# Kernel tuning notes

Hardware: AMD Instinct MI355X
Metric: run time of the kernel (lower is better)

The kernel has to match this reference:

```python
import jax, jax.numpy as jnp
import numpy as np

B, T, D, H, LORA = 4, 1024, 1024, 16, 64
HD = D // H
BLOCK_ID, N_BLOCKS = 6, 12


def _ln(x, w, b, eps=1e-5):
    m = x.mean(-1, keepdims=True)
    v = ((x - m) ** 2).mean(-1, keepdims=True)
    return (x - m) * jax.lax.rsqrt(v + eps) * w + b


def _lora(z, a, b, l):
    return l + jnp.tanh(z @ a.T) @ b.T


def setup_inputs() -> dict:
    key = jax.random.key(0)
    ks = iter(jax.random.split(key, 64))
    rn = lambda shape, s: jax.random.normal(next(ks), shape, jnp.float32) * s
    inp = {}
    inp['x'] = rn((B, T, D), 1.0)
    r1 = 1.0 - BLOCK_ID / N_BLOCKS
    i = np.arange(D)
    inp['xw'] = jnp.asarray(1.0 - (i / D) ** r1, jnp.float32)
    for nm in ('rW', 'kW', 'vW', 'gW'):
        inp[nm] = rn((D, D), 0.02)
    for p in ('r', 'k', 'v', 'g', 'd'):
        inp[p + '_la'] = rn((LORA, D), 0.001)
        inp[p + '_lb'] = rn((D, LORA), 0.001)
        inp[p + '_ll'] = rn((D,), 1.0)
    inp['ln_w'] = jnp.full((HD,), ((1 + BLOCK_ID) / N_BLOCKS) ** 0.7, jnp.float32)
    inp['ln_b'] = jnp.zeros((HD,), jnp.float32)
    inp['oW'] = rn((D, D), 0.02)
    inp['init_state'] = rn((H, HD, HD), 1.0)
    r0 = BLOCK_ID / (N_BLOCKS - 1)
    ih = i % HD
    inp['u'] = jnp.asarray(r0 * (1 - ih / (D - 1)) + np.remainder(0.1 * (ih + 1), 3.0), jnp.float32)
    return inp


def reference(x, xw, rW, kW, vW, gW, r_la, r_lb, r_ll, k_la, k_lb, k_ll,
              v_la, v_lb, v_ll, g_la, g_lb, g_ll, d_la, d_lb, d_ll,
              ln_w, ln_b, oW, init_state, u):
    b, t, d = x.shape
    h = init_state.shape[0]
    hd = d // h
    # token shift: xx[t] = x[t-1], xx[0] = 0
    xx = jnp.concatenate([jnp.zeros_like(x[:, :1]), x[:, :-1]], axis=1)
    dx = xx - x
    lerpx = x + dx * xw
    r = (x + dx * _lora(lerpx, r_la, r_lb, r_ll)) @ rW.T
    k = (x + dx * _lora(lerpx, k_la, k_lb, k_ll)) @ kW.T
    v = (x + dx * _lora(lerpx, v_la, v_lb, v_ll)) @ vW.T
    g = (x + dx * _lora(lerpx, g_la, g_lb, g_ll)) @ gW.T
    w = jnp.exp(-jnp.exp(_lora(x + dx * _lora(lerpx, d_la, d_lb, d_ll), d_la, d_lb, d_ll)))
    # [B,T,D] -> [T,B,H,hd] for the time scan
    split = lambda z: z.reshape(b, t, h, hd).transpose(1, 0, 2, 3)
    rs, ws, ks, vs = split(r), split(w), split(k), split(v)
    uh = u.reshape(h, hd)
    st0 = jnp.broadcast_to(init_state, (b, h, hd, hd))

    def step(st, inp):
        rt, wt, kt, vt = inp
        kv = jnp.einsum('bhi,bhj->bhij', kt, vt)      # outer product
        y = jnp.einsum('bhi,bhij->bhj', rt, st + uh[None, :, :, None] * kv)
        return wt[..., None] * st + kv, y             # diag(w) @ S + kv

    st1, ys = jax.lax.scan(step, st0, (rs, ws, ks, vs))  # ys: [T,B,H,hd]
    o = jax.nn.silu(g.reshape(b, t, h, hd)) * _ln(ys.transpose(1, 0, 2, 3), ln_w, ln_b)
    return o.reshape(b, t, d) @ oW.T, st1
```

## Files before the change

### kernel.cpp

```cpp
#include <hip/hip_runtime.h>
#include <hip/hip_bf16.h>

typedef unsigned short u16;
typedef unsigned int u32;
typedef __attribute__((ext_vector_type(4))) float f32x4;
typedef __attribute__((ext_vector_type(8))) short s16x8;

#define AS1 __attribute__((address_space(1)))
#define AS3 __attribute__((address_space(3)))

#define NB 4
#define TTOK 1024
#define DD 1024
#define NH 16
#define HD 64
#define MT 4096
#define NCH 16
#define CLEN 64

static __device__ __forceinline__ float b2f(u16 u) {
  union { unsigned int u; float f; } c; c.u = ((unsigned int)u) << 16; return c.f;
}
static __device__ __forceinline__ u16 f2b(float f) {
  union { float f; unsigned int u; } c; c.f = f;
  return (u16)((c.u + 0x7fffu + ((c.u >> 16) & 1u)) >> 16);
}
static __device__ __forceinline__ float rdl(float v, int i) {
  union { float f; int s; } c; c.f = v;
  union { int s; float f; } o; o.s = __builtin_amdgcn_readlane(c.s, i);
  return o.f;
}
static __device__ __forceinline__ void gload16(const u16* g, u16* l) {
  __builtin_amdgcn_global_load_lds((const AS1 u32*)g, (AS3 u32*)l, 16, 0, 0);
}
static __device__ __forceinline__ int swz(int lin) {
  return lin ^ (((lin >> 9) & 3) << 5) ^ (((lin >> 7) & 1) << 4);
}

__global__ __launch_bounds__(256) void convW(const float* __restrict__ s0, const float* __restrict__ s1,
                                             const float* __restrict__ s2, const float* __restrict__ s3,
                                             const float* __restrict__ s4, u16* __restrict__ dst) {
  long f = ((long)blockIdx.x * 256 + threadIdx.x) << 2;
  int sel = (int)(f >> 20);
  const float* s = sel == 0 ? s0 : sel == 1 ? s1 : sel == 2 ? s2 : sel == 3 ? s3 : s4;
  long off = f & 1048575;
  f32x4 v = *(const f32x4*)&s[off];
  ushort4 o; o.x = f2b(v[0]); o.y = f2b(v[1]); o.z = f2b(v[2]); o.w = f2b(v[3]);
  *(ushort4*)&dst[f] = o;
}

__global__ __launch_bounds__(256) void convLora(
    const float* a0, const float* a1, const float* a2, const float* a3, const float* a4,
    const float* b0, const float* b1, const float* b2, const float* b3, const float* b4,
    const float* l0, const float* l1, const float* l2, const float* l3, const float* l4,
    u16* __restrict__ laD, u16* __restrict__ lbD, float* __restrict__ llD) {
  long f = ((long)blockIdx.x * 256 + threadIdx.x) << 2;
  if (f < 327680) {
    int sel = (int)(f >> 16); long off = f & 65535;
    const float* s = sel == 0 ? a0 : sel == 1 ? a1 : sel == 2 ? a2 : sel == 3 ? a3 : a4;
    f32x4 v = *(const f32x4*)&s[off];
    ushort4 o; o.x = f2b(v[0]); o.y = f2b(v[1]); o.z = f2b(v[2]); o.w = f2b(v[3]);
    *(ushort4*)&laD[f] = o;
  } else if (f < 655360) {
    long g = f - 327680;
    int sel = (int)(g >> 16); long off = g & 65535;
    const float* s = sel == 0 ? b0 : sel == 1 ? b1 : sel == 2 ? b2 : sel == 3 ? b3 : b4;
    f32x4 v = *(const f32x4*)&s[off];
    ushort4 o; o.x = f2b(v[0]); o.y = f2b(v[1]); o.z = f2b(v[2]); o.w = f2b(v[3]);
    *(ushort4*)&lbD[g] = o;
  } else if (f < 660480) {
    long g = f - 655360;
    int sel = (int)(g >> 10); long off = g & 1023;
    const float* s = sel == 0 ? l0 : sel == 1 ? l1 : sel == 2 ? l2 : sel == 3 ? l3 : l4;
    *(f32x4*)&llD[g] = *(const f32x4*)&s[off];
  }
}

__global__ __launch_bounds__(256) void prep(const float* __restrict__ x, const float* __restrict__ xw,
                                            u16* __restrict__ lerpx, float* __restrict__ dxP) {
  long f = ((long)blockIdx.x * 256 + threadIdx.x) << 2;
  int d = (int)(f & (DD - 1));
  int m = (int)(f >> 10);
  int t = m & (TTOK - 1);
  f32x4 xv = *(const f32x4*)&x[f];
  f32x4 xm = {};
  if (t > 0) xm = *(const f32x4*)&x[f - DD];
  f32x4 xwv = *(const f32x4*)&xw[d];
  f32x4 dx = xm - xv;
  f32x4 lp = xv + dx * xwv;
  *(f32x4*)&dxP[f] = dx;
  ushort4 o; o.x = f2b(lp[0]); o.y = f2b(lp[1]); o.z = f2b(lp[2]); o.w = f2b(lp[3]);
  *(ushort4*)&lerpx[f] = o;
}

template<int BM, int BN, int EPI>
__launch_bounds__(256)
__global__ void gemm2(const u16* __restrict__ Ab, long sAz,
                      const u16* __restrict__ Bb, long sBz,
                      void* __restrict__ Ob, long sOz,
                      const float* __restrict__ llb,
                      const float* __restrict__ xP,
                      const float* __restrict__ dxP,
                      int M, int N, int K) {
  __shared__ __align__(16) u16 As[BM * 64];
  __shared__ __align__(16) u16 Bs[BN * 64];
  const int z = blockIdx.z;
  const u16* A = Ab + (long)z * sAz;
  const u16* Bw = Bb + (long)z * sBz;
  const int m0 = blockIdx.y * BM;
  const int n0 = blockIdx.x * BN;
  const int tid = threadIdx.x;
  const int l = tid & 63;
  const int wv = tid >> 6;
  constexpr int WM = BM / 2, WN = BN / 2;
  constexpr int FM = WM / 16, FN = WN / 16;
  const int wm0 = (wv >> 1) * WM, wn0 = (wv & 1) * WN;
  const int lrow = l & 15, lk = (l >> 4) * 8;
  constexpr int GA = BM / 32, GB = BN / 32;
  int gA[GA], gB[GB];
#pragma unroll
  for (int q = 0; q < GA; ++q) {
    int d = (q * 256 + tid) * 16;
    int bb = swz(d);
    gA[q] = (m0 + (bb >> 7)) * K + ((bb & 127) >> 1);
  }
#pragma unroll
  for (int q = 0; q < GB; ++q) {
    int d = (q * 256 + tid) * 16;
    int bb = swz(d);
    gB[q] = (n0 + (bb >> 7)) * K + ((bb & 127) >> 1);
  }
  int aOff[FM][2], bOff[FN][2];
#pragma unroll
  for (int m = 0; m < FM; ++m)
#pragma unroll
    for (int kk = 0; kk < 2; ++kk)
      aOff[m][kk] = swz(((wm0 + m * 16 + lrow) << 7) + (kk << 6) + (lk << 1));
#pragma unroll
  for (int n = 0; n < FN; ++n)
#pragma unroll
    for (int kk = 0; kk < 2; ++kk)
      bOff[n][kk] = swz(((wn0 + n * 16 + lrow) << 7) + (kk << 6) + (lk << 1));
  f32x4 acc[FM][FN] = {};
  for (int k0 = 0; k0 < K; k0 += 64) {
    __syncthreads();
#pragma unroll
    for (int q = 0; q < GA; ++q)
      gload16(&A[(long)gA[q] + k0], (u16*)((char*)As + (q * 256 + tid) * 16));
#pragma unroll
    for (int q = 0; q < GB; ++q)
      gload16(&Bw[(long)gB[q] + k0], (u16*)((char*)Bs + (q * 256 + tid) * 16));
    __syncthreads();
#pragma unroll
    for (int kk = 0; kk < 2; ++kk) {
      s16x8 af[FM], bfr[FN];
#pragma unroll
      for (int m = 0; m < FM; ++m) af[m] = *(const s16x8*)((const char*)As + aOff[m][kk]);
#pragma unroll
      for (int n = 0; n < FN; ++n) bfr[n] = *(const s16x8*)((const char*)Bs + bOff[n][kk]);
#pragma unroll
      for (int m = 0; m < FM; ++m)
#pragma unroll
        for (int n = 0; n < FN; ++n)
          acc[m][n] = __builtin_amdgcn_mfma_f32_16x16x32_bf16(af[m], bfr[n], acc[m][n], 0, 0, 0);
    }
  }
#pragma unroll
  for (int m = 0; m < FM; ++m) {
#pragma unroll
    for (int n = 0; n < FN; ++n) {
      const int j = n0 + wn0 + n * 16 + lrow;
#pragma unroll
      for (int q = 0; q < 4; ++q) {
        const int i = m0 + wm0 + m * 16 + (l >> 4) * 4 + q;
        const long off = (long)i * N + j;
        float v = acc[m][n][q];
        if constexpr (EPI == 0) {
          ((float*)Ob + (long)z * sOz)[off] = v;
        } else if constexpr (EPI == 1) {
          ((u16*)Ob + (long)z * sOz)[off] = f2b(tanhf(v));
        } else if constexpr (EPI == 2) {
          float val = xP[off] + dxP[off] * (llb[(long)z * N + j] + v);
          ((u16*)Ob + (long)z * sOz)[off] = f2b(val);
        } else if constexpr (EPI == 3) {
          ((float*)Ob + (long)z * sOz)[off] = expf(-expf(llb[j] + v));
        } else {
          ((u16*)Ob + (long)z * sOz)[off] = f2b(v);
        }
      }
    }
  }
}

__global__ __launch_bounds__(128) void scan_local(
    const u16* __restrict__ rP, const u16* __restrict__ kP,
    const u16* __restrict__ vP, const float* __restrict__ wP,
    const float* __restrict__ uP, float* __restrict__ ys0, float* __restrict__ ys1,
    u16* __restrict__ rtil, float* __restrict__ SL, float* __restrict__ AC) {
  const int bhc = blockIdx.x;
  const int c = bhc & (NCH - 1), h = (bhc >> 4) & (NH - 1), b = bhc >> 8;
  const int j = threadIdx.x & 63;
  const int h2 = threadIdx.x >> 6;
  float s[32];
#pragma unroll
  for (int x = 0; x < 32; ++x) s[x] = 0.f;
  float Aj = 1.f;
  const float uj = uP[h * HD + j];
  long base = ((long)(b * TTOK + c * CLEN) << 10) + h * HD;
  float rj = b2f(rP[base + j]), kj = b2f(kP[base + j]);
  float vj = b2f(vP[base + j]), wj = wP[base + j];
  for (int tt = 0; tt < CLEN; ++tt) {
    const long nbase = base + DD;
    float rn = 0.f, kn = 0.f, vn = 0.f, wn = 0.f;
    if (tt + 1 < CLEN) {
      rn = b2f(rP[nbase + j]); kn = b2f(kP[nbase + j]);
      vn = b2f(vP[nbase + j]); wn = wP[nbase + j];
    }
    float ya = 0.f, yb = 0.f;
    if (h2 == 0) {
      rtil[base + j] = f2b(rj * Aj);
#pragma unroll
      for (int x = 0; x < 32; x += 2) {
        { const float ri = rdl(rj, x), ki = rdl(kj, x), wi = rdl(wj, x);
          ya = fmaf(ri, s[x], ya); s[x] = fmaf(wi, s[x], ki * vj); }
        { const float ri = rdl(rj, x + 1), ki = rdl(kj, x + 1), wi = rdl(wj, x + 1);
          yb = fmaf(ri, s[x + 1], yb); s[x + 1] = fmaf(wi, s[x + 1], ki * vj); }
      }
      ys0[base + j] = ya + yb;
    } else {
      float al = rj * uj * kj;
#pragma unroll
      for (int msk = 1; msk < 64; msk <<= 1) al += __shfl_xor(al, msk, 64);
      ya = al * vj;
#pragma unroll
      for (int x = 0; x < 32; x += 2) {
        { const float ri = rdl(rj, 32 + x), ki = rdl(kj, 32 + x), wi = rdl(wj, 32 + x);
          ya = fmaf(ri, s[x], ya); s[x] = fmaf(wi, s[x], ki * vj); }
        { const float ri = rdl(rj, 33 + x), ki = rdl(kj, 33 + x), wi = rdl(wj, 33 + x);
          yb = fmaf(ri, s[x + 1], yb); s[x + 1] = fmaf(wi, s[x + 1], ki * vj); }
      }
      ys1[base + j] = ya + yb;
    }
    Aj *= wj;
    base = nbase;
    rj = rn; kj = kn; vj = vn; wj = wn;
  }
#pragma unroll
  for (int x = 0; x < 32; ++x)
    SL[((long)bhc * 64 + h2 * 32 + x) * 64 + j] = s[x];
  if (h2 == 0) AC[(long)bhc * 64 + j] = Aj;
}

__global__ __launch_bounds__(256) void scan_prop(
    float* __restrict__ SL, const float* __restrict__ AC,
    const float* __restrict__ initS, float* __restrict__ st1) {
  const int bh = blockIdx.x;
  const int h = bh & (NH - 1);
  const int tid = threadIdx.x;
  const int i = tid >> 2, jg = (tid & 3) * 16;
  f32x4 sin4[4];
  const f32x4* ip = (const f32x4*)(initS + ((long)h * 64 + i) * 64 + jg);
#pragma unroll
  for (int e = 0; e < 4; ++e) sin4[e] = ip[e];
  for (int cc = 0; cc < NCH; ++cc) {
    const long bhc = (long)bh * NCH + cc;
    f32x4* slp = (f32x4*)(SL + (bhc * 64 + i) * 64 + jg);
    const float Ai = AC[bhc * 64 + i];
    f32x4 sl4[4];
#pragma unroll
    for (int e = 0; e < 4; ++e) sl4[e] = slp[e];
#pragma unroll
    for (int e = 0; e < 4; ++e) slp[e] = sin4[e];
#pragma unroll
    for (int e = 0; e < 4; ++e) sin4[e] = Ai * sin4[e] + sl4[e];
  }
  f32x4* op = (f32x4*)(st1 + ((long)bh * 64 + i) * 64 + jg);
#pragma unroll
  for (int e = 0; e < 4; ++e) op[e] = sin4[e];
}

__global__ __launch_bounds__(256) void scan_corr(
    const float* __restrict__ SL, const u16* __restrict__ rtil, float* __restrict__ ys) {
  __shared__ __align__(16) float S[64 * 64];
  const int bhc = blockIdx.x;
  const int c = bhc & (NCH - 1), h = (bhc >> 4) & (NH - 1), b = bhc >> 8;
  const int tid = threadIdx.x;
  const f32x4* sp = (const f32x4*)(SL + (long)bhc * 4096);
  for (int q = tid; q < 1024; q += 256) ((f32x4*)S)[q] = sp[q];
  __syncthreads();
  const int t = tid >> 2, jg = (tid & 3) * 16;
  const long base = ((long)(b * TTOK + c * CLEN + t) * DD) + h * HD;
  f32x4 yacc[4] = {};
  const u16* rp = rtil + base;
#pragma unroll 8
  for (int i = 0; i < 64; ++i) {
    const float r = b2f(rp[i]);
    const f32x4* srow = (const f32x4*)&S[i * 64 + jg];
#pragma unroll
    for (int e = 0; e < 4; ++e) yacc[e] += r * srow[e];
  }
  f32x4* yp = (f32x4*)(ys + base + jg);
#pragma unroll
  for (int e = 0; e < 4; ++e) yp[e] += yacc[e];
}

__global__ __launch_bounds__(256) void ln_silu(
    const float* __restrict__ ys0, const float* __restrict__ ys1,
    const u16* __restrict__ gP,
    const float* __restrict__ lnw, const float* __restrict__ lnb,
    u16* __restrict__ oB) {
  const int ridx = blockIdx.x * 4 + (threadIdx.x >> 6);
  const int lane = threadIdx.x & 63;
  const long basem = (long)ridx * 64;
  const float y = ys0[basem + lane] + ys1[basem + lane];
  float su = y, sq = y * y;
#pragma unroll
  for (int msk = 1; msk < 64; msk <<= 1) {
    su += __shfl_xor(su, msk, 64);
    sq += __shfl_xor(sq, msk, 64);
  }
  const float mean = su * (1.f / 64.f);
  const float var = sq * (1.f / 64.f) - mean * mean;
  const float rs = rsqrtf(var + 1e-5f);
  const float g = b2f(gP[basem + lane]);
  const float silu = g / (1.f + expf(-g));
  const float val = silu * ((y - mean) * rs * lnw[lane] + lnb[lane]);
  oB[basem + lane] = f2b(val);
}

extern "C" void kernel_launch(void* const* d_in, const int* in_sizes, int n_in,
                              void* d_out, int out_size, void* d_ws, size_t ws_size,
                              hipStream_t stream) {
  const float* x   = (const float*)d_in[0];
  const float* xw  = (const float*)d_in[1];
  const float* rW  = (const float*)d_in[2];
  const float* kW  = (const float*)d_in[3];
  const float* vW  = (const float*)d_in[4];
  const float* gW  = (const float*)d_in[5];
  const float* r_la = (const float*)d_in[6],  *r_lb = (const float*)d_in[7],  *r_ll = (const float*)d_in[8];
  const float* k_la = (const float*)d_in[9],  *k_lb = (const float*)d_in[10], *k_ll = (const float*)d_in[11];
  const float* v_la = (const float*)d_in[12], *v_lb = (const float*)d_in[13], *v_ll = (const float*)d_in[14];
  const float* g_la = (const float*)d_in[15], *g_lb = (const float*)d_in[16], *g_ll = (const float*)d_in[17];
  const float* d_la = (const float*)d_in[18], *d_lb = (const float*)d_in[19], *d_ll = (const float*)d_in[20];
  const float* lnw = (const float*)d_in[21];
  const float* lnb = (const float*)d_in[22];
  const float* oW  = (const float*)d_in[23];
  const float* initS = (const float*)d_in[24];
  const float* uP  = (const float*)d_in[25];
  float* out = (float*)d_out;

  char* ws = (char*)d_ws;
  u16*   W_all  = (u16*)(ws + 0);
  u16*   la_all = (u16*)(ws + 10485760);
  u16*   lb_all = (u16*)(ws + 11141120);
  float* ll_all = (float*)(ws + 11796480);
  u16*   lerpx  = (u16*)(ws + 11816960);
  float* dxP    = (float*)(ws + 20205568);
  float* ys1    = (float*)(ws + 20205568);
  u16*   t1_all = (u16*)(ws + 36982784);
  u16*   z_all  = (u16*)(ws + 39604224);
  u16*   rkvg   = (u16*)(ws + 81547264);
  float* wbuf   = (float*)(ws + 115101696);
  u16*   rtil   = (u16*)(ws + 131878912);
  float* SL     = (float*)(ws + 140267520);
  float* AC     = (float*)(ws + 157044736);
  float* ys     = (float*)(ws + 157306880);
  u16*   oB     = (u16*)(ws + 174084096);

  convW<<<5120, 256, 0, stream>>>(rW, kW, vW, gW, oW, W_all);
  convLora<<<645, 256, 0, stream>>>(r_la, k_la, v_la, g_la, d_la,
                                    r_lb, k_lb, v_lb, g_lb, d_lb,
                                    r_ll, k_ll, v_ll, g_ll, d_ll,
                                    la_all, lb_all, ll_all);
  prep<<<4096, 256, 0, stream>>>(x, xw, lerpx, dxP);

  gemm2<64, 64, 1><<<dim3(1, 64, 5), 256, 0, stream>>>(
      lerpx, 0L, la_all, 65536L, (void*)t1_all, 262144L, nullptr, nullptr, nullptr, MT, 64, 1024);
  gemm2<128, 128, 2><<<dim3(8, 32, 5), 256, 0, stream>>>(
      t1_all, 262144L, lb_all, 65536L, (void*)z_all, 4194304L, ll_all, x, dxP, MT, 1024, 64);
  gemm2<64, 64, 1><<<dim3(1, 64, 1), 256, 0, stream>>>(
      z_all + 4L * 4194304, 0L, la_all + 4L * 65536, 0L, (void*)t1_all, 0L, nullptr, nullptr, nullptr, MT, 64, 1024);
  gemm2<128, 128, 3><<<dim3(8, 32, 1), 256, 0, stream>>>(
      t1_all, 0L, lb_all + 4L * 65536, 0L, (void*)wbuf, 0L, ll_all + 4096, nullptr, nullptr, MT, 1024, 64);
  gemm2<128, 128, 4><<<dim3(8, 32, 4), 256, 0, stream>>>(
      z_all, 4194304L, W_all, 1048576L, (void*)rkvg, 4194304L, nullptr, nullptr, nullptr, MT, 1024, 1024);

  scan_local<<<1024, 128, 0, stream>>>(rkvg, rkvg + 4194304L, rkvg + 2L * 4194304, wbuf,
                                       uP, ys, ys1, rtil, SL, AC);
  scan_prop<<<64, 256, 0, stream>>>(SL, AC, initS, out + 4194304);
  scan_corr<<<1024, 256, 0, stream>>>(SL, rtil, ys);

  ln_silu<<<16384, 256, 0, stream>>>(ys, ys1, rkvg + 3L * 4194304, lnw, lnb, oB);
  gemm2<128, 128, 0><<<dim3(8, 32, 1), 256, 0, stream>>>(
      oB, 0L, W_all + 4L * 1048576, 0L, (void*)out, 0L, nullptr, nullptr, nullptr, MT, 1024, 1024);
}
```

Before: 399.3 us.

## Split chunk scan across four waves and store x/dx in bf16

The chunk-local scan now uses four wavefronts per block, each owning 16 state rows. Each wave loads its r/k/w slice directly per timestep instead of broadcasting values through readlane, and writes a partial y to one of four buffers that ln_silu sums. scan_prop is split across four times more blocks, and prep writes x and dx as bf16 rather than fp32 to cut epilogue traffic in the LoRA GEMM. In exchange there is more redundant global loading, extra partial-output buffers that alias reused workspace regions, and a small precision loss on x and dx.

```diff
diff --git a/kernel.cpp b/kernel.cpp
--- a/kernel.cpp
+++ b/kernel.cpp
@@ -21,14 +21,12 @@
 static __device__ __forceinline__ float b2f(u16 u) {
   union { unsigned int u; float f; } c; c.u = ((unsigned int)u) << 16; return c.f;
 }
+static __device__ __forceinline__ float ubit(u32 u) {
+  union { u32 u; float f; } c; c.u = u; return c.f;
+}
 static __device__ __forceinline__ u16 f2b(float f) {
   union { float f; unsigned int u; } c; c.f = f;
   return (u16)((c.u + 0x7fffu + ((c.u >> 16) & 1u)) >> 16);
-}
-static __device__ __forceinline__ float rdl(float v, int i) {
-  union { float f; int s; } c; c.f = v;
-  union { int s; float f; } o; o.s = __builtin_amdgcn_readlane(c.s, i);
-  return o.f;
 }
 static __device__ __forceinline__ void gload16(const u16* g, u16* l) {
   __builtin_amdgcn_global_load_lds((const AS1 u32*)g, (AS3 u32*)l, 16, 0, 0);
@@ -77,7 +75,8 @@
 }
 
 __global__ __launch_bounds__(256) void prep(const float* __restrict__ x, const float* __restrict__ xw,
-                                            u16* __restrict__ lerpx, float* __restrict__ dxP) {
+                                            u16* __restrict__ lerpx, u16* __restrict__ xB,
+                                            u16* __restrict__ dxB) {
   long f = ((long)blockIdx.x * 256 + threadIdx.x) << 2;
   int d = (int)(f & (DD - 1));
   int m = (int)(f >> 10);
@@ -88,9 +87,12 @@
   f32x4 xwv = *(const f32x4*)&xw[d];
   f32x4 dx = xm - xv;
   f32x4 lp = xv + dx * xwv;
-  *(f32x4*)&dxP[f] = dx;
   ushort4 o; o.x = f2b(lp[0]); o.y = f2b(lp[1]); o.z = f2b(lp[2]); o.w = f2b(lp[3]);
   *(ushort4*)&lerpx[f] = o;
+  ushort4 ox; ox.x = f2b(xv[0]); ox.y = f2b(xv[1]); ox.z = f2b(xv[2]); ox.w = f2b(xv[3]);
+  *(ushort4*)&xB[f] = ox;
+  ushort4 od; od.x = f2b(dx[0]); od.y = f2b(dx[1]); od.z = f2b(dx[2]); od.w = f2b(dx[3]);
+  *(ushort4*)&dxB[f] = od;
 }
 
 template<int BM, int BN, int EPI>
@@ -99,8 +101,8 @@
                       const u16* __restrict__ Bb, long sBz,
                       void* __restrict__ Ob, long sOz,
                       const float* __restrict__ llb,
-                      const float* __restrict__ xP,
-                      const float* __restrict__ dxP,
+                      const u16* __restrict__ xB,
+                      const u16* __restrict__ dxB,
                       int M, int N, int K) {
   __shared__ __align__(16) u16 As[BM * 64];
   __shared__ __align__(16) u16 Bs[BN * 64];
@@ -180,7 +182,7 @@
         } else if constexpr (EPI == 1) {
           ((u16*)Ob + (long)z * sOz)[off] = f2b(tanhf(v));
         } else if constexpr (EPI == 2) {
-          float val = xP[off] + dxP[off] * (llb[(long)z * N + j] + v);
+          float val = b2f(xB[off]) + b2f(dxB[off]) * (llb[(long)z * N + j] + v);
           ((u16*)Ob + (long)z * sOz)[off] = f2b(val);
         } else if constexpr (EPI == 3) {
           ((float*)Ob + (long)z * sOz)[off] = expf(-expf(llb[j] + v));
@@ -192,91 +194,104 @@
   }
 }
 
-__global__ __launch_bounds__(128) void scan_local(
+__global__ __launch_bounds__(256) void scan_local(
     const u16* __restrict__ rP, const u16* __restrict__ kP,
     const u16* __restrict__ vP, const float* __restrict__ wP,
-    const float* __restrict__ uP, float* __restrict__ ys0, float* __restrict__ ys1,
+    const float* __restrict__ uP,
+    float* __restrict__ ys0, float* __restrict__ ys1,
+    float* __restrict__ ys2, float* __restrict__ ys3,
     u16* __restrict__ rtil, float* __restrict__ SL, float* __restrict__ AC) {
   const int bhc = blockIdx.x;
   const int c = bhc & (NCH - 1), h = (bhc >> 4) & (NH - 1), b = bhc >> 8;
   const int j = threadIdx.x & 63;
-  const int h2 = threadIdx.x >> 6;
-  float s[32];
-#pragma unroll
-  for (int x = 0; x < 32; ++x) s[x] = 0.f;
+  const int qu = __builtin_amdgcn_readfirstlane(threadIdx.x >> 6);
+  const int so = qu * 16;
+  float s[16];
+#pragma unroll
+  for (int x = 0; x < 16; ++x) s[x] = 0.f;
+  long base = ((long)(b * TTOK + c * CLEN) << 10) + h * HD;
+  float* __restrict__ ysel = qu == 0 ? ys0 : qu == 1 ? ys1 : qu == 2 ? ys2 : ys3;
+
+  u32 rc[8], kc[8]; float wc[16];
+#pragma unroll
+  for (int e = 0; e < 8; ++e) {
+    rc[e] = *(const u32*)(rP + base + so + 2 * e);
+    kc[e] = *(const u32*)(kP + base + so + 2 * e);
+  }
+#pragma unroll
+  for (int e = 0; e < 16; ++e) wc[e] = wP[base + so + e];
+
   float Aj = 1.f;
   const float uj = uP[h * HD + j];
-  long base = ((long)(b * TTOK + c * CLEN) << 10) + h * HD;
-  float rj = b2f(rP[base + j]), kj = b2f(kP[base + j]);
-  float vj = b2f(vP[base + j]), wj = wP[base + j];
+  float vjc = b2f(vP[base + j]);
+  float rjv = 0.f, kjv = 0.f, wjv = 0.f;
+  if (qu == 0) { rjv = b2f(rP[base + j]); kjv = b2f(kP[base + j]); wjv = wP[base + j]; }
+
   for (int tt = 0; tt < CLEN; ++tt) {
-    const long nbase = base + DD;
-    float rn = 0.f, kn = 0.f, vn = 0.f, wn = 0.f;
-    if (tt + 1 < CLEN) {
-      rn = b2f(rP[nbase + j]); kn = b2f(kP[nbase + j]);
-      vn = b2f(vP[nbase + j]); wn = wP[nbase + j];
+    const long nb = base + DD;
+    u32 rn_[8], kn_[8]; float wn_[16];
+#pragma unroll
+    for (int e = 0; e < 8; ++e) {
+      rn_[e] = *(const u32*)(rP + nb + so + 2 * e);
+      kn_[e] = *(const u32*)(kP + nb + so + 2 * e);
     }
+#pragma unroll
+    for (int e = 0; e < 16; ++e) wn_[e] = wP[nb + so + e];
+    float vjn = b2f(vP[nb + j]);
+    float rjn = 0.f, kjn = 0.f, wjn = 0.f;
+    if (qu == 0) { rjn = b2f(rP[nb + j]); kjn = b2f(kP[nb + j]); wjn = wP[nb + j]; }
+
     float ya = 0.f, yb = 0.f;
-    if (h2 == 0) {
-      rtil[base + j] = f2b(rj * Aj);
-#pragma unroll
-      for (int x = 0; x < 32; x += 2) {
-        { const float ri = rdl(rj, x), ki = rdl(kj, x), wi = rdl(wj, x);
-          ya = fmaf(ri, s[x], ya); s[x] = fmaf(wi, s[x], ki * vj); }
-        { const float ri = rdl(rj, x + 1), ki = rdl(kj, x + 1), wi = rdl(wj, x + 1);
-          yb = fmaf(ri, s[x + 1], yb); s[x + 1] = fmaf(wi, s[x + 1], ki * vj); }
-      }
-      ys0[base + j] = ya + yb;
-    } else {
-      float al = rj * uj * kj;
+#pragma unroll
+    for (int e = 0; e < 8; ++e) {
+      const float r0 = ubit(rc[e] << 16), r1 = ubit(rc[e] & 0xffff0000u);
+      const float k0 = ubit(kc[e] << 16), k1 = ubit(kc[e] & 0xffff0000u);
+      ya = fmaf(r0, s[2 * e], ya);
+      s[2 * e] = fmaf(wc[2 * e], s[2 * e], k0 * vjc);
+      yb = fmaf(r1, s[2 * e + 1], yb);
+      s[2 * e + 1] = fmaf(wc[2 * e + 1], s[2 * e + 1], k1 * vjc);
+    }
+    float y = ya + yb;
+    if (qu == 0) {
+      rtil[base + j] = f2b(rjv * Aj);
+      float al = rjv * uj * kjv;
 #pragma unroll
       for (int msk = 1; msk < 64; msk <<= 1) al += __shfl_xor(al, msk, 64);
-      ya = al * vj;
-#pragma unroll
-      for (int x = 0; x < 32; x += 2) {
-        { const float ri = rdl(rj, 32 + x), ki = rdl(kj, 32 + x), wi = rdl(wj, 32 + x);
-          ya = fmaf(ri, s[x], ya); s[x] = fmaf(wi, s[x], ki * vj); }
-        { const float ri = rdl(rj, 33 + x), ki = rdl(kj, 33 + x), wi = rdl(wj, 33 + x);
-          yb = fmaf(ri, s[x + 1], yb); s[x + 1] = fmaf(wi, s[x + 1], ki * vj); }
-      }
-      ys1[base + j] = ya + yb;
+      y = fmaf(al, vjc, y);
+      Aj *= wjv;
+      rjv = rjn; kjv = kjn; wjv = wjn;
     }
-    Aj *= wj;
-    base = nbase;
-    rj = rn; kj = kn; vj = vn; wj = wn;
-  }
-#pragma unroll
-  for (int x = 0; x < 32; ++x)
-    SL[((long)bhc * 64 + h2 * 32 + x) * 64 + j] = s[x];
-  if (h2 == 0) AC[(long)bhc * 64 + j] = Aj;
+    ysel[base + j] = y;
+    base = nb; vjc = vjn;
+#pragma unroll
+    for (int e = 0; e < 8; ++e) { rc[e] = rn_[e]; kc[e] = kn_[e]; }
+#pragma unroll
+    for (int e = 0; e < 16; ++e) wc[e] = wn_[e];
+  }
+#pragma unroll
+  for (int x = 0; x < 16; ++x)
+    SL[((long)bhc * 64 + so + x) * 64 + j] = s[x];
+  if (qu == 0) AC[(long)bhc * 64 + j] = Aj;
 }
 
 __global__ __launch_bounds__(256) void scan_prop(
     float* __restrict__ SL, const float* __restrict__ AC,
     const float* __restrict__ initS, float* __restrict__ st1) {
-  const int bh = blockIdx.x;
+  const int bh = blockIdx.x >> 2;
+  const int jq = blockIdx.x & 3;
   const int h = bh & (NH - 1);
-  const int tid = threadIdx.x;
-  const int i = tid >> 2, jg = (tid & 3) * 16;
-  f32x4 sin4[4];
-  const f32x4* ip = (const f32x4*)(initS + ((long)h * 64 + i) * 64 + jg);
-#pragma unroll
-  for (int e = 0; e < 4; ++e) sin4[e] = ip[e];
+  const int i = threadIdx.x >> 2;
+  const int jo = jq * 16 + (threadIdx.x & 3) * 4;
+  f32x4 sin4 = *(const f32x4*)(initS + ((long)h * 64 + i) * 64 + jo);
   for (int cc = 0; cc < NCH; ++cc) {
     const long bhc = (long)bh * NCH + cc;
-    f32x4* slp = (f32x4*)(SL + (bhc * 64 + i) * 64 + jg);
+    f32x4* slp = (f32x4*)(SL + (bhc * 64 + i) * 64 + jo);
     const float Ai = AC[bhc * 64 + i];
-    f32x4 sl4[4];
-#pragma unroll
-    for (int e = 0; e < 4; ++e) sl4[e] = slp[e];
-#pragma unroll
-    for (int e = 0; e < 4; ++e) slp[e] = sin4[e];
-#pragma unroll
-    for (int e = 0; e < 4; ++e) sin4[e] = Ai * sin4[e] + sl4[e];
-  }
-  f32x4* op = (f32x4*)(st1 + ((long)bh * 64 + i) * 64 + jg);
-#pragma unroll
-  for (int e = 0; e < 4; ++e) op[e] = sin4[e];
+    f32x4 sl = *slp;
+    *slp = sin4;
+    sin4 = Ai * sin4 + sl;
+  }
+  *(f32x4*)(st1 + ((long)bh * 64 + i) * 64 + jo) = sin4;
 }
 
 __global__ __launch_bounds__(256) void scan_corr(
@@ -306,13 +321,14 @@
 
 __global__ __launch_bounds__(256) void ln_silu(
     const float* __restrict__ ys0, const float* __restrict__ ys1,
+    const float* __restrict__ ys2, const float* __restrict__ ys3,
     const u16* __restrict__ gP,
     const float* __restrict__ lnw, const float* __restrict__ lnb,
     u16* __restrict__ oB) {
   const int ridx = blockIdx.x * 4 + (threadIdx.x >> 6);
   const int lane = threadIdx.x & 63;
   const long basem = (long)ridx * 64;
-  const float y = ys0[basem + lane] + ys1[basem + lane];
+  const float y = ys0[basem + lane] + ys1[basem + lane] + ys2[basem + lane] + ys3[basem + lane];
   float su = y, sq = y * y;
 #pragma unroll
   for (int msk = 1; msk < 64; msk <<= 1) {
@@ -355,8 +371,8 @@
   u16*   lb_all = (u16*)(ws + 11141120);
   float* ll_all = (float*)(ws + 11796480);
   u16*   lerpx  = (u16*)(ws + 11816960);
-  float* dxP    = (float*)(ws + 20205568);
-  float* ys1    = (float*)(ws + 20205568);
+  u16*   xB     = (u16*)(ws + 20205568);
+  u16*   dxB    = (u16*)(ws + 28594176);
   u16*   t1_all = (u16*)(ws + 36982784);
   u16*   z_all  = (u16*)(ws + 39604224);
   u16*   rkvg   = (u16*)(ws + 81547264);
@@ -364,20 +380,23 @@
   u16*   rtil   = (u16*)(ws + 131878912);
   float* SL     = (float*)(ws + 140267520);
   float* AC     = (float*)(ws + 157044736);
-  float* ys     = (float*)(ws + 157306880);
+  float* ys0    = (float*)(ws + 157306880);
   u16*   oB     = (u16*)(ws + 174084096);
+  float* ys1    = (float*)(ws + 11816960);
+  float* ys2    = (float*)(ws + 39604224);
+  float* ys3    = (float*)(ws + 56381440);
 
   convW<<<5120, 256, 0, stream>>>(rW, kW, vW, gW, oW, W_all);
   convLora<<<645, 256, 0, stream>>>(r_la, k_la, v_la, g_la, d_la,
                                     r_lb, k_lb, v_lb, g_lb, d_lb,
                                     r_ll, k_ll, v_ll, g_ll, d_ll,
                                     la_all, lb_all, ll_all);
-  prep<<<4096, 256, 0, stream>>>(x, xw, lerpx, dxP);
+  prep<<<4096, 256, 0, stream>>>(x, xw, lerpx, xB, dxB);
 
   gemm2<64, 64, 1><<<dim3(1, 64, 5), 256, 0, stream>>>(
       lerpx, 0L, la_all, 65536L, (void*)t1_all, 262144L, nullptr, nullptr, nullptr, MT, 64, 1024);
   gemm2<128, 128, 2><<<dim3(8, 32, 5), 256, 0, stream>>>(
-      t1_all, 262144L, lb_all, 65536L, (void*)z_all, 4194304L, ll_all, x, dxP, MT, 1024, 64);
+      t1_all, 262144L, lb_all, 65536L, (void*)z_all, 4194304L, ll_all, xB, dxB, MT, 1024, 64);
   gemm2<64, 64, 1><<<dim3(1, 64, 1), 256, 0, stream>>>(
       z_all + 4L * 4194304, 0L, la_all + 4L * 65536, 0L, (void*)t1_all, 0L, nullptr, nullptr, nullptr, MT, 64, 1024);
   gemm2<128, 128, 3><<<dim3(8, 32, 1), 256, 0, stream>>>(
@@ -385,12 +404,12 @@
   gemm2<128, 128, 4><<<dim3(8, 32, 4), 256, 0, stream>>>(
       z_all, 4194304L, W_all, 1048576L, (void*)rkvg, 4194304L, nullptr, nullptr, nullptr, MT, 1024, 1024);
 
-  scan_local<<<1024, 128, 0, stream>>>(rkvg, rkvg + 4194304L, rkvg + 2L * 4194304, wbuf,
-                                       uP, ys, ys1, rtil, SL, AC);
-  scan_prop<<<64, 256, 0, stream>>>(SL, AC, initS, out + 4194304);
-  scan_corr<<<1024, 256, 0, stream>>>(SL, rtil, ys);
-
-  ln_silu<<<16384, 256, 0, stream>>>(ys, ys1, rkvg + 3L * 4194304, lnw, lnb, oB);
+  scan_local<<<1024, 256, 0, stream>>>(rkvg, rkvg + 4194304L, rkvg + 2L * 4194304, wbuf,
+                                       uP, ys0, ys1, ys2, ys3, rtil, SL, AC);
+  scan_prop<<<256, 256, 0, stream>>>(SL, AC, initS, out + 4194304);
+  scan_corr<<<1024, 256, 0, stream>>>(SL, rtil, ys0);
+
+  ln_silu<<<16384, 256, 0, stream>>>(ys0, ys1, ys2, ys3, rkvg + 3L * 4194304, lnw, lnb, oB);
   gemm2<128, 128, 0><<<dim3(8, 32, 1), 256, 0, stream>>>(
       oB, 0L, W_all + 4L * 1048576, 0L, (void*)out, 0L, nullptr, nullptr, nullptr, MT, 1024, 1024);
 }
```

Result: faster. 388.4 us (-2.7%).
